# Optimization experiments

Hardware: AMD Instinct MI355X
Metric: run time of the kernel (lower is better)

Reference implementation:

```python
import jax, jax.numpy as jnp
import numpy as np

B, Q, D = 8, 900, 256
NH, DH = 8, 32
FF = 1024
NLEVELS, NPOINTS, NLAYERS = 4, 4, 6
SHAPES = [(100, 100), (50, 50), (25, 25), (13, 13)]
S = sum(h * w for h, w in SHAPES)  # 13294
EPS = 1e-5
SCALE = 1.0 / float(np.sqrt(DH))


def layer_norm(x, g, b):
    mu = jnp.mean(x, -1, keepdims=True)
    var = jnp.var(x, -1, keepdims=True)
    return (x - mu) * jax.lax.rsqrt(var + EPS) * g + b


def mha(x, wi, bi, wo, bo):
    qkv = x @ wi.T + bi
    q, k, v = jnp.split(qkv, 3, axis=-1)
    q = q.reshape(B, Q, NH, DH)
    k = k.reshape(B, Q, NH, DH)
    v = v.reshape(B, Q, NH, DH)
    attn = jax.nn.softmax(jnp.einsum('bqhd,bkhd->bhqk', q, k) * SCALE, -1)
    o = jnp.einsum('bhqk,bkhd->bqhd', attn, v).reshape(B, Q, D)
    return o @ wo.T + bo


def msda_core(value, loc, aw):
    # value (B,S,NH,DH); loc (B,Q,NH,L,P,2) in [0,1]; aw (B,Q,NH,L,P)
    v = value.transpose(0, 2, 1, 3)  # (B,NH,S,DH)
    out = jnp.zeros((B, NH, Q, DH), value.dtype)
    start = 0
    for lvl, (H_, W_) in enumerate(SHAPES):
        vl = v[:, :, start:start + H_ * W_]  # (B,NH,HW,DH)
        start += H_ * W_
        l = loc[:, :, :, lvl].transpose(0, 2, 1, 3, 4).reshape(B, NH, Q * NPOINTS, 2)
        # grid_sample align_corners=False pixel coords
        x = l[..., 0] * W_ - 0.5
        y = l[..., 1] * H_ - 0.5
        x0 = jnp.floor(x)
        y0 = jnp.floor(y)
        wx = x - x0
        wy = y - y0
        g = jnp.zeros((B, NH, Q * NPOINTS, DH), value.dtype)
        for dy, dx, w in ((0, 0, (1 - wx) * (1 - wy)), (0, 1, wx * (1 - wy)),
                          (1, 0, (1 - wx) * wy), (1, 1, wx * wy)):
            xi = x0 + dx
            yi = y0 + dy
            valid = ((xi >= 0) & (xi < W_) & (yi >= 0) & (yi < H_)).astype(value.dtype)
            idx = (jnp.clip(yi, 0, H_ - 1) * W_ + jnp.clip(xi, 0, W_ - 1)).astype(jnp.int32)
            gi = jnp.take_along_axis(vl, idx[..., None], axis=2)  # (B,NH,QP,DH)
            g = g + gi * (w * valid)[..., None]
        g = g.reshape(B, NH, Q, NPOINTS, DH)
        a = aw[:, :, :, lvl].transpose(0, 2, 1, 3)  # (B,NH,Q,P)
        out = out + jnp.einsum('bhqpd,bhqp->bhqd', g, a)
    return out.transpose(0, 2, 1, 3).reshape(B, Q, D)


def msda(query, ref, value_in, vp_w, vp_b, so_w, so_b, aw_w, aw_b, op_w, op_b):
    value = (value_in @ vp_w.T + vp_b).reshape(B, S, NH, DH)
    off = (query @ so_w.T + so_b).reshape(B, Q, NH, NLEVELS, NPOINTS, 2)
    aw = (query @ aw_w.T + aw_b).reshape(B, Q, NH, NLEVELS * NPOINTS)
    aw = jax.nn.softmax(aw, -1).reshape(B, Q, NH, NLEVELS, NPOINTS)
    # offset normalizer is (W, H) per level
    norm = jnp.array([[w, h] for h, w in SHAPES], jnp.float32)
    loc = ref[:, :, None, :, None, :] + off / norm[None, None, None, :, None, :]
    return msda_core(value, loc, aw) @ op_w.T + op_b


def setup_inputs():
    key = jax.random.key(0)
    it = iter(jax.random.split(key, 32))

    def rn(shape, s=0.02):
        return jax.random.normal(next(it), shape, jnp.float32) * s

    z = lambda n: jnp.zeros((n,), jnp.float32)
    o = lambda n: jnp.ones((n,), jnp.float32)
    NOFF = NH * NLEVELS * NPOINTS
    return {
        'tgt': rn((B, Q, D), 1.0),
        'reference_points': jax.random.uniform(next(it), (B, Q, 2), jnp.float32),
        'memory': rn((B, S, D), 1.0),
        'spatial_shapes': jnp.array(SHAPES, jnp.int32),
        'level_start_index': jnp.array(np.cumsum([0] + [h * w for h, w in SHAPES[:-1]]), jnp.int32),
        'valid_ratios': jnp.ones((B, NLEVELS, 2), jnp.float32),
        'query_pos': rn((B, Q, D), 1.0),
        'sa_in_w': rn((3 * D, D)), 'sa_in_b': z(3 * D),
        'sa_out_w': rn((D, D)), 'sa_out_b': z(D),
        'n1_g': o(D), 'n1_b': z(D),
        'n2_g': o(D), 'n2_b': z(D),
        'n3_g': o(D), 'n3_b': z(D),
        'vp_w': rn((D, D)), 'vp_b': z(D),
        'so_w': rn((NOFF * 2, D)), 'so_b': rn((NOFF * 2,), 0.5),
        'aw_w': rn((NOFF, D)), 'aw_b': z(NOFF),
        'op_w': rn((D, D)), 'op_b': z(D),
        'ff1_w': rn((FF, D)), 'ff1_b': z(FF),
        'ff2_w': rn((D, FF)), 'ff2_b': z(D),
    }


def reference(tgt, reference_points, memory, spatial_shapes, level_start_index,
              valid_ratios, query_pos,
              sa_in_w, sa_in_b, sa_out_w, sa_out_b,
              n1_g, n1_b, n2_g, n2_b, n3_g, n3_b,
              vp_w, vp_b, so_w, so_b, aw_w, aw_b, op_w, op_b,
              ff1_w, ff1_b, ff2_w, ff2_b):
    # NOTE: nn.ModuleList([decoder_layer]*num_layers) in the source shares one
    # layer's weights across all 6 layers; bbox_embed is None so reference
    # points are constant across layers.
    output = tgt
    ref_input = reference_points[:, :, None, :] * valid_ratios[:, None, :, :]  # (B,Q,L,2)
    inter, inter_refs = [], []
    for _ in range(NLAYERS):
        output = output + query_pos
        t2 = mha(output, sa_in_w, sa_in_b, sa_out_w, sa_out_b)
        output = layer_norm(output + t2, n1_g, n1_b)
        t2 = msda(output, ref_input, memory, vp_w, vp_b, so_w, so_b, aw_w, aw_b, op_w, op_b)
        output = layer_norm(output + t2, n2_g, n2_b)
        t2 = jax.nn.relu(output @ ff1_w.T + ff1_b) @ ff2_w.T + ff2_b
        output = layer_norm(output + t2, n3_g, n3_b)
        inter.append(output)
        inter_refs.append(reference_points)
    return (jnp.stack(inter), jnp.stack(inter_refs))
```

## Files before the change

kernel.cpp:

```cpp
#include <hip/hip_runtime.h>
#include <hip/hip_bf16.h>

typedef __hip_bfloat16 bf16;
typedef __bf16 bf16x8 __attribute__((ext_vector_type(8)));
typedef float  f32x4  __attribute__((ext_vector_type(4)));

#define NB 8
#define NQ 900
#define DM 256
#define NHEADS 8
#define DHEAD 32
#define NFF 1024
#define NLAY 6
#define NS 13294
#define BQ (NB*NQ)
#define LN_EPS 1e-5f
#define ATT_SCALE 0.17677669529663687f
#define SAK 40
#define VWS 264

__device__ __forceinline__ float bfd(const bf16* p, size_t i){ return __bfloat162float(p[i]); }

__device__ __forceinline__ float ldv(const void* p, size_t i, int mode, bool extF32)
{
    if (mode == 0) return ((const float*)p)[i];
    if (mode == 1) return bfd((const bf16*)p, i);
    return extF32 ? ((const float*)p)[i] : bfd((const bf16*)p, i);
}

__device__ __forceinline__ void unpack8(uint4 u, float* t)
{
    t[0] = __uint_as_float((u.x & 0xffffu) << 16);
    t[1] = __uint_as_float(u.x & 0xffff0000u);
    t[2] = __uint_as_float((u.y & 0xffffu) << 16);
    t[3] = __uint_as_float(u.y & 0xffff0000u);
    t[4] = __uint_as_float((u.z & 0xffffu) << 16);
    t[5] = __uint_as_float(u.z & 0xffff0000u);
    t[6] = __uint_as_float((u.w & 0xffffu) << 16);
    t[7] = __uint_as_float(u.w & 0xffff0000u);
}

__global__ __launch_bounds__(256) void detect_dtype(const void* __restrict__ tgt,
        float* __restrict__ flag)
{
    __shared__ float red[256];
    int t = threadIdx.x;
    const unsigned short* u = (const unsigned short*)tgt;
    float m = 0.f;
    for (int i = t; i < 2048; i += 256) {
        unsigned int bits = ((unsigned int)u[i]) << 16;
        float v = fabsf(__uint_as_float(bits));
        if (!isfinite(v)) v = 1e30f;
        m = fmaxf(m, v);
    }
    red[t] = m;
    __syncthreads();
    for (int st = 128; st; st >>= 1) {
        if (t < st) red[t] = fmaxf(red[t], red[t + st]);
        __syncthreads();
    }
    if (t == 0) flag[0] = (red[0] > 1e8f) ? 1.f : 0.f;
}

__global__ __launch_bounds__(256) void convert_w(const void* __restrict__ src,
        bf16* __restrict__ dst, const float* __restrict__ flagp)
{
    const bool ef = flagp[0] > 0.5f;
    size_t base = ((size_t)blockIdx.x * 256 + threadIdx.x) * 8;
    if (ef) {
        const float* s = (const float*)src + base;
        float4 f0 = *(const float4*)s;
        float4 f1 = *(const float4*)(s + 4);
        union { bf16 a[8]; uint4 u; } t;
        t.a[0] = __float2bfloat16(f0.x); t.a[1] = __float2bfloat16(f0.y);
        t.a[2] = __float2bfloat16(f0.z); t.a[3] = __float2bfloat16(f0.w);
        t.a[4] = __float2bfloat16(f1.x); t.a[5] = __float2bfloat16(f1.y);
        t.a[6] = __float2bfloat16(f1.z); t.a[7] = __float2bfloat16(f1.w);
        *(uint4*)(dst + base) = t.u;
    } else {
        *(uint4*)(dst + base) = *(const uint4*)((const bf16*)src + base);
    }
}

__global__ __launch_bounds__(256) void gemm_vp(const void* __restrict__ A,
        const bf16* __restrict__ Wb, const void* __restrict__ bias,
        bf16* __restrict__ C, int M, const float* __restrict__ flagp)
{
    const bool ef = flagp[0] > 0.5f;
    __shared__ __align__(16) bf16 Wl[256 * VWS];
    __shared__ __align__(16) bf16 Al[32 * VWS];
    const int tid = threadIdx.x;
    const int w = tid >> 6, lane = tid & 63, lm = lane & 15, lq = lane >> 4;
    const int wq = w * 64;

    for (int u = tid; u < 8192; u += 256) {
        int row = u >> 5, col = (u & 31) * 8;
        *(uint4*)&Wl[row * VWS + col] = *(const uint4*)(Wb + (size_t)row * 256 + col);
    }

    float bv[4];
    #pragma unroll
    for (int nt = 0; nt < 4; nt++) bv[nt] = ldv(bias, wq + nt * 16 + lm, 2, ef);

    const int arow_l = tid >> 3;
    const int acol   = (tid & 7) * 32;

    const int ntiles = (M + 31) / 32;
    for (int tile = blockIdx.x; tile < ntiles; tile += gridDim.x) {
        const int m0 = tile * 32;
        __syncthreads();
        {
            const int grow = m0 + arow_l;
            if (grow < M) {
                if (ef) {
                    const float* ap = (const float*)A + (size_t)grow * 256 + acol;
                    #pragma unroll
                    for (int j = 0; j < 4; j++) {
                        float4 f0 = *(const float4*)(ap + j * 8);
                        float4 f1 = *(const float4*)(ap + j * 8 + 4);
                        union { bf16 a[8]; uint4 u; } t;
                        t.a[0] = __float2bfloat16(f0.x); t.a[1] = __float2bfloat16(f0.y);
                        t.a[2] = __float2bfloat16(f0.z); t.a[3] = __float2bfloat16(f0.w);
                        t.a[4] = __float2bfloat16(f1.x); t.a[5] = __float2bfloat16(f1.y);
                        t.a[6] = __float2bfloat16(f1.z); t.a[7] = __float2bfloat16(f1.w);
                        *(uint4*)&Al[arow_l * VWS + acol + j * 8] = t.u;
                    }
                } else {
                    const bf16* ap = (const bf16*)A + (size_t)grow * 256 + acol;
                    #pragma unroll
                    for (int j = 0; j < 4; j++)
                        *(uint4*)&Al[arow_l * VWS + acol + j * 8] =
                            *(const uint4*)(ap + j * 8);
                }
            } else {
                uint4 z = make_uint4(0u, 0u, 0u, 0u);
                #pragma unroll
                for (int j = 0; j < 4; j++)
                    *(uint4*)&Al[arow_l * VWS + acol + j * 8] = z;
            }
        }
        __syncthreads();

        f32x4 acc[2][4];
        #pragma unroll
        for (int mi = 0; mi < 2; mi++)
            #pragma unroll
            for (int nt = 0; nt < 4; nt++)
                acc[mi][nt] = (f32x4){0.f, 0.f, 0.f, 0.f};

        #pragma unroll
        for (int ks = 0; ks < 8; ks++) {
            bf16x8 af[2];
            #pragma unroll
            for (int mi = 0; mi < 2; mi++)
                af[mi] = *(const bf16x8*)&Al[(mi * 16 + lm) * VWS + ks * 32 + lq * 8];
            #pragma unroll
            for (int nt = 0; nt < 4; nt++) {
                bf16x8 bfr = *(const bf16x8*)&Wl[(wq + nt * 16 + lm) * VWS + ks * 32 + lq * 8];
                #pragma unroll
                for (int mi = 0; mi < 2; mi++)
                    acc[mi][nt] = __builtin_amdgcn_mfma_f32_16x16x32_bf16(
                                      af[mi], bfr, acc[mi][nt], 0, 0, 0);
            }
        }

        #pragma unroll
        for (int mi = 0; mi < 2; mi++) {
            #pragma unroll
            for (int r = 0; r < 4; r++) {
                int m = m0 + mi * 16 + lq * 4 + r;
                if (m >= M) continue;
                #pragma unroll
                for (int nt = 0; nt < 4; nt++) {
                    int col = wq + nt * 16 + lm;
                    C[(size_t)m * 256 + col] = __float2bfloat16(acc[mi][nt][r] + bv[nt]);
                }
            }
        }
    }
}

__device__ __forceinline__ void stage_a32(bf16* As, const void* A, bool a_bf16,
        int m0, int M, int K, int k0, int tid)
{
    const int row = tid >> 3, col = (tid & 7) * 4;
    const int arow = m0 + row;
    union { bf16 a[4]; uint2 u; } t;
    if (arow < M) {
        size_t base = (size_t)arow * K + k0 + col;
        if (a_bf16) {
            t.u = *(const uint2*)((const bf16*)A + base);
        } else {
            float4 f = *(const float4*)((const float*)A + base);
            t.a[0] = __float2bfloat16(f.x); t.a[1] = __float2bfloat16(f.y);
            t.a[2] = __float2bfloat16(f.z); t.a[3] = __float2bfloat16(f.w);
        }
    } else {
        t.u = make_uint2(0u, 0u);
    }
    *(uint2*)&As[row * SAK + col] = t.u;
}

__global__ __launch_bounds__(256) void gemm_a(const void* __restrict__ A, int amode,
        const bf16* __restrict__ Wb, const void* __restrict__ bias,
        void* __restrict__ C, int cmode, int M, int N, int K, int relu,
        const float* __restrict__ flagp)
{
    const bool ef = flagp[0] > 0.5f;
    const bool a_bf16 = (amode == 1) || (amode == 2 && !ef);
    __shared__ __align__(16) bf16 As[32 * SAK];
    __shared__ __align__(16) bf16 Ws[256 * SAK];
    const int tid = threadIdx.x;
    const int m0 = blockIdx.y * 32, n0 = blockIdx.x * 256;
    const int w = tid >> 6, lane = tid & 63, lm = lane & 15, lq = lane >> 4;
    const int wr = w >> 1, wc = w & 1;
    const int srow = tid >> 2, scol = (tid & 3) * 8;

    f32x4 acc[8];
    #pragma unroll
    for (int nt = 0; nt < 8; nt++) acc[nt] = (f32x4){0.f, 0.f, 0.f, 0.f};

    for (int k0 = 0; k0 < K; k0 += 32) {
        stage_a32(As, A, a_bf16, m0, M, K, k0, tid);
        #pragma unroll
        for (int it = 0; it < 4; it++) {
            int rr = it * 64 + srow;
            *(uint4*)&Ws[rr * SAK + scol] =
                *(const uint4*)(Wb + (size_t)(n0 + rr) * K + k0 + scol);
        }
        __syncthreads();

        bf16x8 af = *(const bf16x8*)&As[(wr * 16 + lm) * SAK + lq * 8];
        #pragma unroll
        for (int nt = 0; nt < 8; nt++) {
            bf16x8 bfr = *(const bf16x8*)&Ws[(wc * 128 + nt * 16 + lm) * SAK + lq * 8];
            acc[nt] = __builtin_amdgcn_mfma_f32_16x16x32_bf16(af, bfr, acc[nt], 0, 0, 0);
        }
        __syncthreads();
    }

    #pragma unroll
    for (int nt = 0; nt < 8; nt++) {
        int n = n0 + wc * 128 + nt * 16 + lm;
        float bv = ldv(bias, n, 2, ef);
        #pragma unroll
        for (int r = 0; r < 4; r++) {
            int m = m0 + wr * 16 + lq * 4 + r;
            if (m >= M) continue;
            float v = acc[nt][r] + bv;
            if (relu) v = fmaxf(v, 0.f);
            size_t ci = (size_t)m * N + n;
            if (cmode == 0) ((float*)C)[ci] = v;
            else            ((bf16*)C)[ci] = __float2bfloat16(v);
        }
    }
}

__global__ __launch_bounds__(256) void gemm_ln(const bf16* __restrict__ A,
        const bf16* __restrict__ Wb, const void* __restrict__ bias,
        const float* __restrict__ res, const void* __restrict__ gw,
        const void* __restrict__ bw, float* __restrict__ out32,
        bf16* __restrict__ outbf, void* __restrict__ dout, size_t obase,
        const void* __restrict__ qp, int M, int K,
        const float* __restrict__ flagp)
{
    const bool ef = flagp[0] > 0.5f;
    __shared__ __align__(16) bf16 As[32 * SAK];
    __shared__ __align__(16) bf16 Ws[256 * SAK];
    const int tid = threadIdx.x;
    const int m0 = blockIdx.y * 32;
    const int w = tid >> 6, lane = tid & 63, lm = lane & 15, lq = lane >> 4;
    const int wr = w >> 1, wc = w & 1;
    const int srow = tid >> 2, scol = (tid & 3) * 8;

    f32x4 acc[8];
    #pragma unroll
    for (int nt = 0; nt < 8; nt++) acc[nt] = (f32x4){0.f, 0.f, 0.f, 0.f};

    for (int k0 = 0; k0 < K; k0 += 32) {
        stage_a32(As, A, true, m0, M, K, k0, tid);
        #pragma unroll
        for (int it = 0; it < 4; it++) {
            int rr = it * 64 + srow;
            *(uint4*)&Ws[rr * SAK + scol] =
                *(const uint4*)(Wb + (size_t)rr * K + k0 + scol);
        }
        __syncthreads();

        bf16x8 af = *(const bf16x8*)&As[(wr * 16 + lm) * SAK + lq * 8];
        #pragma unroll
        for (int nt = 0; nt < 8; nt++) {
            bf16x8 bfr = *(const bf16x8*)&Ws[(wc * 128 + nt * 16 + lm) * SAK + lq * 8];
            acc[nt] = __builtin_amdgcn_mfma_f32_16x16x32_bf16(af, bfr, acc[nt], 0, 0, 0);
        }
        __syncthreads();
    }

    float bias_c[8], gcol[8], bcol[8];
    #pragma unroll
    for (int nt = 0; nt < 8; nt++) {
        int col = wc * 128 + nt * 16 + lm;
        bias_c[nt] = ldv(bias, col, 2, ef);
        gcol[nt]   = ldv(gw,   col, 2, ef);
        bcol[nt]   = ldv(bw,   col, 2, ef);
    }
    #pragma unroll
    for (int r = 0; r < 4; r++) {
        int row = m0 + wr * 16 + lq * 4 + r;
        bool vr_ = row < M;
        #pragma unroll
        for (int nt = 0; nt < 8; nt++) {
            int col = wc * 128 + nt * 16 + lm;
            float rv = vr_ ? res[(size_t)row * DM + col] : 0.f;
            acc[nt][r] += bias_c[nt] + rv;
        }
    }

    float* red = (float*)As;
    float mu[4], rstd[4];
    #pragma unroll
    for (int r = 0; r < 4; r++) {
        float s = 0.f;
        #pragma unroll
        for (int nt = 0; nt < 8; nt++) s += acc[nt][r];
        s += __shfl_xor(s, 1, 64); s += __shfl_xor(s, 2, 64);
        s += __shfl_xor(s, 4, 64); s += __shfl_xor(s, 8, 64);
        if (lm == 0) red[(wr * 16 + lq * 4 + r) * 2 + wc] = s;
    }
    __syncthreads();
    #pragma unroll
    for (int r = 0; r < 4; r++) {
        int rl = wr * 16 + lq * 4 + r;
        mu[r] = (red[rl * 2] + red[rl * 2 + 1]) * (1.f / DM);
    }
    #pragma unroll
    for (int r = 0; r < 4; r++) {
        float q = 0.f;
        #pragma unroll
        for (int nt = 0; nt < 8; nt++) {
            float d = acc[nt][r] - mu[r];
            q += d * d;
        }
        q += __shfl_xor(q, 1, 64); q += __shfl_xor(q, 2, 64);
        q += __shfl_xor(q, 4, 64); q += __shfl_xor(q, 8, 64);
        if (lm == 0) red[64 + (wr * 16 + lq * 4 + r) * 2 + wc] = q;
    }
    __syncthreads();
    #pragma unroll
    for (int r = 0; r < 4; r++) {
        int rl = wr * 16 + lq * 4 + r;
        float var = (red[64 + rl * 2] + red[64 + rl * 2 + 1]) * (1.f / DM);
        rstd[r] = rsqrtf(var + LN_EPS);
    }

    #pragma unroll
    for (int r = 0; r < 4; r++) {
        int row = m0 + wr * 16 + lq * 4 + r;
        if (row >= M) continue;
        size_t rbase = (size_t)row * DM;
        #pragma unroll
        for (int nt = 0; nt < 8; nt++) {
            int col = wc * 128 + nt * 16 + lm;
            float o = (acc[nt][r] - mu[r]) * rstd[r] * gcol[nt] + bcol[nt];
            if (dout) {
                if (ef) ((float*)dout)[obase + rbase + col] = o;
                else    ((bf16*)dout)[obase + rbase + col] = __float2bfloat16(o);
            }
            float o2 = o + (qp ? ldv(qp, rbase + col, 2, ef) : 0.f);
            out32[rbase + col] = o2;
            outbf[rbase + col] = __float2bfloat16(o2);
        }
    }
}

__global__ __launch_bounds__(256) void gemm_soaw(const bf16* __restrict__ A,
        const bf16* __restrict__ Wb, const void* __restrict__ b1,
        const void* __restrict__ b2, float* __restrict__ C1,
        float* __restrict__ C2, int M, const float* __restrict__ flagp)
{
    const bool ef = flagp[0] > 0.5f;
    const int K = DM;
    __shared__ __align__(16) bf16 As[32 * SAK];
    __shared__ __align__(16) bf16 Ws[128 * SAK];
    const int tid = threadIdx.x;
    const int m0 = blockIdx.y * 32, n0 = blockIdx.x * 128;
    const int w = tid >> 6, lane = tid & 63, lm = lane & 15, lq = lane >> 4;
    const int wr = w >> 1, wc = w & 1;
    const int srow = tid >> 2, scol = (tid & 3) * 8;

    f32x4 acc[4];
    #pragma unroll
    for (int nt = 0; nt < 4; nt++) acc[nt] = (f32x4){0.f, 0.f, 0.f, 0.f};

    for (int k0 = 0; k0 < K; k0 += 32) {
        stage_a32(As, A, true, m0, M, K, k0, tid);
        #pragma unroll
        for (int it = 0; it < 2; it++) {
            int rr = it * 64 + srow;
            *(uint4*)&Ws[rr * SAK + scol] =
                *(const uint4*)(Wb + (size_t)(n0 + rr) * K + k0 + scol);
        }
        __syncthreads();

        bf16x8 af = *(const bf16x8*)&As[(wr * 16 + lm) * SAK + lq * 8];
        #pragma unroll
        for (int nt = 0; nt < 4; nt++) {
            bf16x8 bfr = *(const bf16x8*)&Ws[(wc * 64 + nt * 16 + lm) * SAK + lq * 8];
            acc[nt] = __builtin_amdgcn_mfma_f32_16x16x32_bf16(af, bfr, acc[nt], 0, 0, 0);
        }
        __syncthreads();
    }

    float* Cd; const void* bsrc; int nst, c0;
    if (n0 < 256) { Cd = C1; bsrc = b1; nst = 256; c0 = n0; }
    else          { Cd = C2; bsrc = b2; nst = 128; c0 = n0 - 256; }

    #pragma unroll
    for (int nt = 0; nt < 4; nt++) {
        int cl = wc * 64 + nt * 16 + lm;
        float bv = ldv(bsrc, c0 + cl, 2, ef);
        #pragma unroll
        for (int r = 0; r < 4; r++) {
            int m = m0 + wr * 16 + lq * 4 + r;
            if (m >= M) continue;
            Cd[(size_t)m * nst + c0 + cl] = acc[nt][r] + bv;
        }
    }
}

__global__ __launch_bounds__(256) void add_qpos(const void* __restrict__ a, int amode,
        const void* __restrict__ qp, float* __restrict__ o, bf16* __restrict__ ob,
        const float* __restrict__ flagp)
{
    const bool ef = flagp[0] > 0.5f;
    int i = blockIdx.x * 256 + threadIdx.x;
    float v = ldv(a, i, amode, ef) + ldv(qp, i, 2, ef);
    o[i]  = v;
    ob[i] = __float2bfloat16(v);
}

__global__ __launch_bounds__(256) void mha_mfma(const bf16* __restrict__ qkv,
        bf16* __restrict__ out)
{
    const int qt = blockIdx.x, h = blockIdx.y, b = blockIdx.z;
    const int q0 = qt * 64;
    const int tid = threadIdx.x;
    const int w = tid >> 6, lane = tid & 63;
    const int lm = lane & 15, lq = lane >> 4;
    const int srow = tid >> 2, sc = (tid & 3) * 8;

    __shared__ __align__(16) bf16 Qs[64][SAK];
    __shared__ __align__(16) bf16 Ks[64][SAK];
    __shared__ __align__(16) bf16 Vt[32][66];
    __shared__ __align__(16) bf16 Pt[64][66];

    const bf16* base = qkv + (size_t)b * NQ * 768;

    {
        bf16 tmp[8];
        if (q0 + srow < NQ) {
            uint4 u = *(const uint4*)(base + (size_t)(q0 + srow) * 768 + h * DHEAD + sc);
            float t[8]; unpack8(u, t);
            #pragma unroll
            for (int i = 0; i < 8; i++) tmp[i] = __float2bfloat16(t[i] * ATT_SCALE);
        } else {
            #pragma unroll
            for (int i = 0; i < 8; i++) tmp[i] = __float2bfloat16(0.f);
        }
        *(uint4*)&Qs[srow][sc] = *(const uint4*)tmp;
    }
    __syncthreads();
    const bf16x8 qf = *(const bf16x8*)&Qs[w * 16 + lm][lq * 8];

    f32x4 O[2] = {{0.f,0.f,0.f,0.f},{0.f,0.f,0.f,0.f}};
    float mrow = -1e30f, lrow = 0.f;

    for (int k0 = 0; k0 < NQ; k0 += 64) {
        __syncthreads();
        {
            uint4 uk = {0u,0u,0u,0u}, uv = {0u,0u,0u,0u};
            if (k0 + srow < NQ) {
                const bf16* rp = base + (size_t)(k0 + srow) * 768 + h * DHEAD + sc;
                uk = *(const uint4*)(rp + 256);
                uv = *(const uint4*)(rp + 512);
            }
            *(uint4*)&Ks[srow][sc] = uk;
            const bf16* vv = (const bf16*)&uv;
            #pragma unroll
            for (int i = 0; i < 8; i++) Vt[sc + i][srow] = vv[i];
        }
        __syncthreads();

        float sv[16];
        #pragma unroll
        for (int mt = 0; mt < 4; mt++) {
            bf16x8 kf = *(const bf16x8*)&Ks[mt * 16 + lm][lq * 8];
            f32x4 d = __builtin_amdgcn_mfma_f32_16x16x32_bf16(kf, qf,
                        (f32x4){0.f,0.f,0.f,0.f}, 0, 0, 0);
            sv[mt*4+0] = d[0]; sv[mt*4+1] = d[1]; sv[mt*4+2] = d[2]; sv[mt*4+3] = d[3];
        }
        #pragma unroll
        for (int mt = 0; mt < 4; mt++)
            #pragma unroll
            for (int r = 0; r < 4; r++)
                if (k0 + mt * 16 + lq * 4 + r >= NQ) sv[mt*4+r] = -1e30f;

        float tmax = sv[0];
        #pragma unroll
        for (int j = 1; j < 16; j++) tmax = fmaxf(tmax, sv[j]);
        tmax = fmaxf(tmax, __shfl_xor(tmax, 16, 64));
        tmax = fmaxf(tmax, __shfl_xor(tmax, 32, 64));
        float mnew = fmaxf(mrow, tmax);
        float alpha = __expf(mrow - mnew);
        mrow = mnew;
        float psum = 0.f;
        #pragma unroll
        for (int j = 0; j < 16; j++) {
            float p = __expf(sv[j] - mnew);
            sv[j] = p; psum += p;
        }
        psum += __shfl_xor(psum, 16, 64);
        psum += __shfl_xor(psum, 32, 64);
        lrow = lrow * alpha + psum;

        #pragma unroll
        for (int mt = 0; mt < 4; mt++)
            #pragma unroll
            for (int r = 0; r < 4; r++)
                Pt[mt * 16 + lq * 4 + r][w * 16 + lm] = __float2bfloat16(sv[mt*4+r]);

        #pragma unroll
        for (int mt = 0; mt < 2; mt++)
            #pragma unroll
            for (int r = 0; r < 4; r++) O[mt][r] *= alpha;
        #pragma unroll
        for (int ks = 0; ks < 2; ks++) {
            union { bf16 a[8]; bf16x8 v; } pf;
            #pragma unroll
            for (int j = 0; j < 8; j++)
                pf.a[j] = Pt[ks * 32 + lq * 8 + j][w * 16 + lm];
            #pragma unroll
            for (int mt = 0; mt < 2; mt++) {
                bf16x8 vf = *(const bf16x8*)&Vt[mt * 16 + lm][ks * 32 + lq * 8];
                O[mt] = __builtin_amdgcn_mfma_f32_16x16x32_bf16(vf, pf.v, O[mt], 0, 0, 0);
            }
        }
    }

    int q = q0 + w * 16 + lm;
    if (q < NQ) {
        float invl = 1.f / lrow;
        bf16* op = out + ((size_t)(b * NQ + q)) * DM + h * DHEAD;
        #pragma unroll
        for (int mt = 0; mt < 2; mt++)
            #pragma unroll
            for (int r = 0; r < 4; r++)
                op[mt * 16 + lq * 4 + r] = __float2bfloat16(O[mt][r] * invl);
    }
}

__global__ __launch_bounds__(256) void msda_sample8(const bf16* __restrict__ value,
        const float* __restrict__ off, const float* __restrict__ aw,
        const void* __restrict__ refp, const void* __restrict__ vr,
        bf16* __restrict__ out, const float* __restrict__ flagp)
{
    const bool ef = flagp[0] > 0.5f;
    const int tid = threadIdx.x;
    const int bq0 = blockIdx.x * 8;

    __shared__ float sOff[8][256];
    __shared__ float sAw[8][128];
    __shared__ float sref[8][2];
    __shared__ float svrq[8][8];

    {
        const float* osrc = off + (size_t)bq0 * 256;
        #pragma unroll
        for (int i = 0; i < 2; i++) {
            int e = i * 1024 + tid * 4;
            *(float4*)&sOff[e >> 8][e & 255] = *(const float4*)(osrc + e);
        }
        int e2 = tid * 4;
        *(float4*)&sAw[e2 >> 7][e2 & 127] = *(const float4*)(aw + (size_t)bq0 * 128 + e2);
    }
    if (tid < 16) sref[tid >> 1][tid & 1] = ldv(refp, (size_t)(bq0 + (tid >> 1)) * 2 + (tid & 1), 2, ef);
    if (tid < 64) {
        int qi = tid >> 3, j = tid & 7;
        int b = (bq0 + qi) / NQ;
        svrq[qi][j] = ldv(vr, b * 8 + j, 2, ef);
    }
    __syncthreads();

    if (tid < 64) {
        int qi = tid >> 3, h = tid & 7;
        float* p = &sAw[qi][h * 16];
        float mx = -1e30f;
        #pragma unroll
        for (int j = 0; j < 16; j++) mx = fmaxf(mx, p[j]);
        float s = 0.f;
        #pragma unroll
        for (int j = 0; j < 16; j++) { float e = __expf(p[j] - mx); p[j] = e; s += e; }
        float inv = 1.f / s;
        #pragma unroll
        for (int j = 0; j < 16; j++) p[j] *= inv;
    }
    __syncthreads();

    const int qi = tid >> 5, sub = tid & 31;
    const int h = sub >> 2, cg = sub & 3;
    const int bq = bq0 + qi;
    const int b = bq / NQ;
    const bf16* vb = value + (size_t)b * NS * DM + h * DHEAD + cg * 8;

    float acc[8];
    #pragma unroll
    for (int j = 0; j < 8; j++) acc[j] = 0.f;

    const int HS[4] = {100, 50, 25, 13};
    const int ST[4] = {0, 10000, 12500, 13125};
    #pragma unroll
    for (int lvl = 0; lvl < 4; lvl++) {
        const int W_ = HS[lvl], H_ = HS[lvl], st = ST[lvl];
        float rx = sref[qi][0] * svrq[qi][lvl * 2 + 0] * (float)W_;
        float ry = sref[qi][1] * svrq[qi][lvl * 2 + 1] * (float)H_;
        #pragma unroll
        for (int p = 0; p < 4; p++) {
            int oi = h * 32 + lvl * 8 + p * 2;
            float x = fminf(fmaxf(rx + sOff[qi][oi]     - 0.5f, -4.f), (float)W_ + 4.f);
            float y = fminf(fmaxf(ry + sOff[qi][oi + 1] - 0.5f, -4.f), (float)H_ + 4.f);
            float x0f = floorf(x), y0f = floorf(y);
            float wx = x - x0f, wy = y - y0f;
            int x0 = (int)x0f, y0 = (int)y0f;
            int x1i = x0 + 1, y1i = y0 + 1;
            bool vx0 = (x0 >= 0) && (x0 < W_), vx1 = (x1i >= 0) && (x1i < W_);
            bool vy0 = (y0 >= 0) && (y0 < H_), vy1 = (y1i >= 0) && (y1i < H_);
            float g[8];
            #pragma unroll
            for (int j = 0; j < 8; j++) g[j] = 0.f;
            float t[8];
            if (vy0) {
                int rowo = (st + y0 * W_) * DM;
                if (vx0) {
                    uint4 u = *(const uint4*)(vb + rowo + x0 * DM);
                    unpack8(u, t);
                    float wgt = (1.f - wx) * (1.f - wy);
                    #pragma unroll
                    for (int j = 0; j < 8; j++) g[j] += wgt * t[j];
                }
                if (vx1) {
                    uint4 u = *(const uint4*)(vb + rowo + x1i * DM);
                    unpack8(u, t);
                    float wgt = wx * (1.f - wy);
                    #pragma unroll
                    for (int j = 0; j < 8; j++) g[j] += wgt * t[j];
                }
            }
            if (vy1) {
                int rowo = (st + y1i * W_) * DM;
                if (vx0) {
                    uint4 u = *(const uint4*)(vb + rowo + x0 * DM);
                    unpack8(u, t);
                    float wgt = (1.f - wx) * wy;
                    #pragma unroll
                    for (int j = 0; j < 8; j++) g[j] += wgt * t[j];
                }
                if (vx1) {
                    uint4 u = *(const uint4*)(vb + rowo + x1i * DM);
                    unpack8(u, t);
                    float wgt = wx * wy;
                    #pragma unroll
                    for (int j = 0; j < 8; j++) g[j] += wgt * t[j];
                }
            }
            float a = sAw[qi][h * 16 + lvl * 4 + p];
            #pragma unroll
            for (int j = 0; j < 8; j++) acc[j] += a * g[j];
        }
    }

    union { bf16 t[8]; uint4 u; } pk;
    #pragma unroll
    for (int j = 0; j < 8; j++) pk.t[j] = __float2bfloat16(acc[j]);
    *(uint4*)(out + (size_t)bq * DM + h * DHEAD + cg * 8) = pk.u;
}

__global__ __launch_bounds__(256) void copy_refs(const void* __restrict__ refp,
        void* __restrict__ out, const float* __restrict__ flagp)
{
    const bool ef = flagp[0] > 0.5f;
    int i = blockIdx.x * 256 + threadIdx.x;
    if (i >= NLAY * BQ * 2) return;
    float v = ldv(refp, i % (BQ * 2), 2, ef);
    size_t oi = (size_t)NLAY * BQ * DM + i;
    if (ef) ((float*)out)[oi] = v;
    else    ((bf16*)out)[oi] = __float2bfloat16(v);
}

extern "C" void kernel_launch(void* const* d_in, const int* in_sizes, int n_in,
                              void* d_out, int out_size, void* d_ws, size_t ws_size,
                              hipStream_t stream)
{
    const void* tgt     = d_in[0];
    const void* refp    = d_in[1];
    const void* memory  = d_in[2];
    const void* vr      = d_in[5];
    const void* qp      = d_in[6];
    const void* sa_in_w = d_in[7];
    const void* sa_in_b = d_in[8];
    const void* sa_out_w= d_in[9];
    const void* sa_out_b= d_in[10];
    const void* n1_g    = d_in[11];
    const void* n1_b    = d_in[12];
    const void* n2_g    = d_in[13];
    const void* n2_b    = d_in[14];
    const void* n3_g    = d_in[15];
    const void* n3_b    = d_in[16];
    const void* vp_w    = d_in[17];
    const void* vp_b    = d_in[18];
    const void* so_w    = d_in[19];
    const void* so_b    = d_in[20];
    const void* aw_w    = d_in[21];
    const void* aw_b    = d_in[22];
    const void* op_w    = d_in[23];
    const void* op_b    = d_in[24];
    const void* ff1_w   = d_in[25];
    const void* ff1_b   = d_in[26];
    const void* ff2_w   = d_in[27];
    const void* ff2_b   = d_in[28];

    char* w = (char*)d_ws;
    float* flagp  = (float*)w;  w += 256;
    bf16*  value  = (bf16*)w;   w += (size_t)NB * NS * DM * 2;
    float* outbuf = (float*)w;  w += (size_t)BQ * DM * 4;
    float* x1samp = (float*)w;  w += (size_t)BQ * DM * 4;
    bf16*  bigb   = (bf16*)w;   w += (size_t)BQ * NFF * 2;
    float* attoff = (float*)w;  w += (size_t)BQ * DM * 4;
    float* awb    = (float*)w;  w += (size_t)BQ * 128 * 4;
    bf16*  abuf   = (bf16*)w;   w += (size_t)BQ * DM * 2;
    bf16*  outbf  = (bf16*)w;   w += (size_t)BQ * DM * 2;
    bf16* wb_sa_in = (bf16*)w;  w += (size_t)768 * 256 * 2;
    bf16* wb_sa_out= (bf16*)w;  w += (size_t)256 * 256 * 2;
    bf16* wb_soaw  = (bf16*)w;  w += (size_t)384 * 256 * 2;
    bf16* wb_op    = (bf16*)w;  w += (size_t)256 * 256 * 2;
    bf16* wb_ff1   = (bf16*)w;  w += (size_t)NFF * 256 * 2;
    bf16* wb_ff2   = (bf16*)w;  w += (size_t)256 * NFF * 2;
    bf16* wb_vp    = (bf16*)w;  w += (size_t)256 * 256 * 2;

    const int gy = (BQ + 31) / 32;
    const int MV = NB * NS;

    detect_dtype<<<1, 256, 0, stream>>>(tgt, flagp);
    convert_w<<< 96, 256, 0, stream>>>(sa_in_w,  wb_sa_in,  flagp);
    convert_w<<< 32, 256, 0, stream>>>(sa_out_w, wb_sa_out, flagp);
    convert_w<<< 32, 256, 0, stream>>>(so_w,     wb_soaw,   flagp);
    convert_w<<< 16, 256, 0, stream>>>(aw_w,     wb_soaw + 256 * 256, flagp);
    convert_w<<< 32, 256, 0, stream>>>(op_w,     wb_op,     flagp);
    convert_w<<<128, 256, 0, stream>>>(ff1_w,    wb_ff1,    flagp);
    convert_w<<<128, 256, 0, stream>>>(ff2_w,    wb_ff2,    flagp);
    convert_w<<< 32, 256, 0, stream>>>(vp_w,     wb_vp,     flagp);

    gemm_vp<<<256, 256, 0, stream>>>(memory, wb_vp, vp_b, value, MV, flagp);

    copy_refs<<<(NLAY * BQ * 2 + 255) / 256, 256, 0, stream>>>(refp, d_out, flagp);

    add_qpos<<<BQ * DM / 256, 256, 0, stream>>>(tgt, 2, qp, x1samp, abuf, flagp);

    for (int l = 0; l < NLAY; l++) {
        gemm_a<<<dim3(768/256, gy), 256, 0, stream>>>(
            abuf, 1, wb_sa_in, sa_in_b, bigb, 1, BQ, 768, DM, 0, flagp);
        mha_mfma<<<dim3(15, NHEADS, NB), 256, 0, stream>>>(bigb, abuf);
        gemm_ln<<<dim3(1, gy), 256, 0, stream>>>(
            abuf, wb_sa_out, sa_out_b, x1samp, n1_g, n1_b,
            outbuf, outbf, nullptr, 0, nullptr, BQ, DM, flagp);

        gemm_soaw<<<dim3(3, gy), 256, 0, stream>>>(
            outbf, wb_soaw, so_b, aw_b, attoff, awb, BQ, flagp);
        msda_sample8<<<BQ / 8, 256, 0, stream>>>(value, attoff, awb, refp, vr, abuf, flagp);
        gemm_ln<<<dim3(1, gy), 256, 0, stream>>>(
            abuf, wb_op, op_b, outbuf, n2_g, n2_b,
            outbuf, outbf, nullptr, 0, nullptr, BQ, DM, flagp);

        gemm_a<<<dim3(NFF/256, gy), 256, 0, stream>>>(
            outbf, 1, wb_ff1, ff1_b, bigb, 1, BQ, NFF, DM, 1, flagp);
        gemm_ln<<<dim3(1, gy), 256, 0, stream>>>(
            bigb, wb_ff2, ff2_b, outbuf, n3_g, n3_b,
            x1samp, abuf, d_out, (size_t)l * BQ * DM, qp, BQ, NFF, flagp);
    }
}
```

Before: 1.527 ms.

## Hold value-projection weights in registers and enlarge M tile to 64 rows

The value-projection GEMM now keeps each wave's slice of the 256x256 weight matrix in registers instead of a 135KB shared-memory copy. That frees LDS, so two blocks can run per CU and the grid grows to 512 blocks. Each tile now covers 64 rows so the register-held weights are reused across more MFMAs. The cost is heavy register pressure (128 VGPRs for weights plus 64 for accumulators), which risks spills under the two-block launch bound.

```diff
diff --git a/kernel.cpp b/kernel.cpp
--- a/kernel.cpp
+++ b/kernel.cpp
@@ -82,90 +82,89 @@
     }
 }
 
-__global__ __launch_bounds__(256) void gemm_vp(const void* __restrict__ A,
+__global__ __launch_bounds__(256, 2) void gemm_vp(const void* __restrict__ A,
         const bf16* __restrict__ Wb, const void* __restrict__ bias,
         bf16* __restrict__ C, int M, const float* __restrict__ flagp)
 {
     const bool ef = flagp[0] > 0.5f;
-    __shared__ __align__(16) bf16 Wl[256 * VWS];
-    __shared__ __align__(16) bf16 Al[32 * VWS];
+    __shared__ __align__(16) bf16 Al[64 * VWS];
     const int tid = threadIdx.x;
     const int w = tid >> 6, lane = tid & 63, lm = lane & 15, lq = lane >> 4;
     const int wq = w * 64;
 
-    for (int u = tid; u < 8192; u += 256) {
-        int row = u >> 5, col = (u & 31) * 8;
-        *(uint4*)&Wl[row * VWS + col] = *(const uint4*)(Wb + (size_t)row * 256 + col);
-    }
+    bf16x8 wf[4][8];
+    #pragma unroll
+    for (int nt = 0; nt < 4; nt++)
+        #pragma unroll
+        for (int ks = 0; ks < 8; ks++)
+            wf[nt][ks] = *(const bf16x8*)(Wb +
+                (size_t)(wq + nt * 16 + lm) * 256 + ks * 32 + lq * 8);
 
     float bv[4];
     #pragma unroll
     for (int nt = 0; nt < 4; nt++) bv[nt] = ldv(bias, wq + nt * 16 + lm, 2, ef);
 
-    const int arow_l = tid >> 3;
-    const int acol   = (tid & 7) * 32;
-
-    const int ntiles = (M + 31) / 32;
+    const int arow_l = tid >> 2;
+    const int asub   = tid & 3;
+
+    const int ntiles = (M + 63) / 64;
     for (int tile = blockIdx.x; tile < ntiles; tile += gridDim.x) {
-        const int m0 = tile * 32;
+        const int m0 = tile * 64;
         __syncthreads();
         {
             const int grow = m0 + arow_l;
             if (grow < M) {
                 if (ef) {
-                    const float* ap = (const float*)A + (size_t)grow * 256 + acol;
+                    const float* ap = (const float*)A + (size_t)grow * 256;
                     #pragma unroll
-                    for (int j = 0; j < 4; j++) {
-                        float4 f0 = *(const float4*)(ap + j * 8);
-                        float4 f1 = *(const float4*)(ap + j * 8 + 4);
-                        union { bf16 a[8]; uint4 u; } t;
-                        t.a[0] = __float2bfloat16(f0.x); t.a[1] = __float2bfloat16(f0.y);
-                        t.a[2] = __float2bfloat16(f0.z); t.a[3] = __float2bfloat16(f0.w);
-                        t.a[4] = __float2bfloat16(f1.x); t.a[5] = __float2bfloat16(f1.y);
-                        t.a[6] = __float2bfloat16(f1.z); t.a[7] = __float2bfloat16(f1.w);
-                        *(uint4*)&Al[arow_l * VWS + acol + j * 8] = t.u;
+                    for (int j = 0; j < 16; j++) {
+                        int colf = j * 16 + asub * 4;
+                        float4 f = *(const float4*)(ap + colf);
+                        union { bf16 a[4]; uint2 u; } t;
+                        t.a[0] = __float2bfloat16(f.x); t.a[1] = __float2bfloat16(f.y);
+                        t.a[2] = __float2bfloat16(f.z); t.a[3] = __float2bfloat16(f.w);
+                        *(uint2*)&Al[arow_l * VWS + colf] = t.u;
                     }
                 } else {
-                    const bf16* ap = (const bf16*)A + (size_t)grow * 256 + acol;
+                    const bf16* ap = (const bf16*)A + (size_t)grow * 256;
                     #pragma unroll
-                    for (int j = 0; j < 4; j++)
-                        *(uint4*)&Al[arow_l * VWS + acol + j * 8] =
-                            *(const uint4*)(ap + j * 8);
+                    for (int j = 0; j < 8; j++) {
+                        int cole = j * 32 + asub * 8;
+                        *(uint4*)&Al[arow_l * VWS + cole] = *(const uint4*)(ap + cole);
+                    }
                 }
             } else {
                 uint4 z = make_uint4(0u, 0u, 0u, 0u);
                 #pragma unroll
-                for (int j = 0; j < 4; j++)
-                    *(uint4*)&Al[arow_l * VWS + acol + j * 8] = z;
+                for (int j = 0; j < 8; j++)
+                    *(uint4*)&Al[arow_l * VWS + j * 32 + asub * 8] = z;
             }
         }
         __syncthreads();
 
-        f32x4 acc[2][4];
-        #pragma unroll
-        for (int mi = 0; mi < 2; mi++)
+        f32x4 acc[4][4];
+        #pragma unroll
+        for (int mi = 0; mi < 4; mi++)
             #pragma unroll
             for (int nt = 0; nt < 4; nt++)
                 acc[mi][nt] = (f32x4){0.f, 0.f, 0.f, 0.f};
 
         #pragma unroll
         for (int ks = 0; ks < 8; ks++) {
-            bf16x8 af[2];
-            #pragma unroll
-            for (int mi = 0; mi < 2; mi++)
+            bf16x8 af[4];
+            #pragma unroll
+            for (int mi = 0; mi < 4; mi++)
                 af[mi] = *(const bf16x8*)&Al[(mi * 16 + lm) * VWS + ks * 32 + lq * 8];
             #pragma unroll
-            for (int nt = 0; nt < 4; nt++) {
-                bf16x8 bfr = *(const bf16x8*)&Wl[(wq + nt * 16 + lm) * VWS + ks * 32 + lq * 8];
+            for (int nt = 0; nt < 4; nt++)
                 #pragma unroll
-                for (int mi = 0; mi < 2; mi++)
+                for (int mi = 0; mi < 4; mi++)
                     acc[mi][nt] = __builtin_amdgcn_mfma_f32_16x16x32_bf16(
-                                      af[mi], bfr, acc[mi][nt], 0, 0, 0);
-            }
-        }
-
-        #pragma unroll
-        for (int mi = 0; mi < 2; mi++) {
+                                      af[mi], wf[nt][ks], acc[mi][nt], 0, 0, 0);
+        }
+
+        #pragma unroll
+        for (int mi = 0; mi < 4; mi++) {
             #pragma unroll
             for (int r = 0; r < 4; r++) {
                 int m = m0 + mi * 16 + lq * 4 + r;
@@ -759,7 +758,7 @@
     convert_w<<<128, 256, 0, stream>>>(ff2_w,    wb_ff2,    flagp);
     convert_w<<< 32, 256, 0, stream>>>(vp_w,     wb_vp,     flagp);
 
-    gemm_vp<<<256, 256, 0, stream>>>(memory, wb_vp, vp_b, value, MV, flagp);
+    gemm_vp<<<512, 256, 0, stream>>>(memory, wb_vp, vp_b, value, MV, flagp);
 
     copy_refs<<<(NLAY * BQ * 2 + 255) / 256, 256, 0, stream>>>(refp, d_out, flagp);
 
```

Result: no change. 1.523 ms (-0.3%).
